# Optimization experiments

Hardware: AMD Instinct MI355X
Metric: run time of the kernel (lower is better)

## Reference

```python
import jax, jax.numpy as jnp
import numpy as np

H, D, VD = 8, 64, 64
QD, KD, VDIM, OUT = 512, 512, 512, 512
N, QS, VS = 16, 512, 512
TEMP = 10.0              # softstair_temp
SCALING = D ** -0.5


def _softstair(x):
    fl = jnp.floor(x)
    return fl + jax.nn.sigmoid(TEMP * (jnp.abs(x - fl) - 0.5))


def setup_inputs() -> dict:
    key = jax.random.key(0)
    ks = jax.random.split(key, 24)
    f = jax.random.normal
    s = 0.03  # xavier-ish scale
    return {
        "Q": f(ks[0], (N, QS, QD), jnp.float32),
        "K": f(ks[1], (N, VS, KD), jnp.float32),
        "V": f(ks[2], (N, VS, VDIM), jnp.float32),
        "past_state": f(ks[3], (N, H, QS, D), jnp.float32),
        "past_attention": jax.random.uniform(ks[4], (N, H, QS, 1), jnp.float32),
        "value_positions": jnp.arange(VS, dtype=jnp.float32),
        "attention_mask": jnp.ones((N, QS, VS), jnp.int32),
        "Wq": f(ks[5], (QD, H * D), jnp.float32) * s,
        "Wk": f(ks[6], (KD, H * D), jnp.float32) * s,
        "Wv": f(ks[7], (VDIM, H * VD), jnp.float32) * s,
        "Wpos": f(ks[8], (QD, H * D), jnp.float32) * s,
        "bpos": f(ks[9], (H * D,), jnp.float32) * s,
        "Wsigma": f(ks[10], (H, D, 1), jnp.float32) * s,
        "Wrho": f(ks[11], (H, D, 3), jnp.float32) * s,
        "mix_w": f(ks[12], (QD, 1), jnp.float32) * s,
        "mix_b": f(ks[13], (1,), jnp.float32) * s,
        "gru_wi": f(ks[14], (D, 3 * D), jnp.float32) * s,
        "gru_wh": f(ks[15], (D, 3 * D), jnp.float32) * s,
        "gru_bi": f(ks[16], (3 * D,), jnp.float32) * s,
        "gru_bh": f(ks[17], (3 * D,), jnp.float32) * s,
        "Wc": f(ks[18], (H * VD, OUT), jnp.float32) * s,
    }


def reference(Q, K, V, past_state, past_attention, value_positions, attention_mask,
              Wq, Wk, Wv, Wpos, bpos, Wsigma, Wrho, mix_w, mix_b,
              gru_wi, gru_wh, gru_bi, gru_bh, Wc):
    n, qS, _ = Q.shape
    vS = K.shape[1]
    mask_f = attention_mask.astype(jnp.float32)          # [N,qS,vS]
    mask_b = attention_mask.astype(bool)[:, None]        # [N,1,qS,vS]
    lengths = jnp.sum(mask_f, axis=-1)                   # [N,qS]
    l_1 = jnp.maximum(1.0, lengths - 1.0)[:, None, :, None]
    step_size = 1.0 / l_1                                # [N,1,qS,1]
    nvp = value_positions[None, None, None, :] * step_size  # [N,1,qS,vS]

    # mix gate
    mix = jax.nn.sigmoid(Q @ mix_w + mix_b)[:, None]     # [N,1,qS,1]

    # projections -> [N,H,S,d]
    Qpos = (Q @ Wpos + bpos).reshape(n, qS, H, D).transpose(0, 2, 1, 3)
    Qh = (Q @ Wq).reshape(n, qS, H, D).transpose(0, 2, 1, 3)
    Kh = (K @ Wk).reshape(n, vS, H, D).transpose(0, 2, 1, 3)
    Vh = (V @ Wv).reshape(n, vS, H, VD).transpose(0, 2, 1, 3)

    # content attention
    content = jnp.einsum('bhqd,bhkd->bhqk', Qh, Kh) * SCALING
    content_attn = jax.nn.softmax(jnp.where(mask_b, content, -jnp.inf), axis=-1)

    # GRUCell update (torch gate order r,z,n) on relu(Qpos) with past_state
    x = jax.nn.relu(Qpos)
    gi = x @ gru_wi + gru_bi
    gh = past_state @ gru_wh + gru_bh
    ir, iz, inn = jnp.split(gi, 3, axis=-1)
    hr, hz, hn = jnp.split(gh, 3, axis=-1)
    r = jax.nn.sigmoid(ir + hr)
    z = jax.nn.sigmoid(iz + hz)
    nn_ = jnp.tanh(inn + r * hn)
    state = (1.0 - z) * nn_ + z * past_state             # [N,H,qS,D]

    # location (Gaussian) attention
    sigma = (jax.nn.relu(jnp.einsum('bhqd,hde->bhqe', state, Wsigma)) + 0.27) \
            / lengths[:, None, :, None]                  # [N,H,qS,1]
    rho = jnp.einsum('bhqd,hde->bhqe', state, Wrho)      # [N,H,qS,3]
    steps = _softstair(rho[..., 0:1])
    attn_gate = jax.nn.sigmoid(rho[..., 1:2])
    bias_gate = jax.nn.sigmoid(rho[..., 2:3])
    mu_ = steps * step_size + attn_gate * past_attention + bias_gate
    # leaky clamp to [0,1]
    mu = jnp.maximum(0.01 * mu_, jnp.minimum(mu_, 1.0 + 0.01 * mu_))
    diff = nvp - mu                                      # [N,H,qS,vS]
    gauss = jnp.exp(-(diff * diff) / (2.0 * sigma * sigma))
    g = gauss * mask_f[:, None]
    pos_attn = g / jnp.sum(g + 1e-20, axis=-1, keepdims=True)

    scores = mix * pos_attn + (1.0 - mix) * content_attn
    attended = jnp.einsum('bhqk,bhkv->bhqv', scores, Vh)
    out = attended.transpose(0, 2, 1, 3).reshape(n, qS, H * VD) @ Wc
    return out
```

## Files before the change

### kernel.cpp

```cpp
#include <hip/hip_runtime.h>


typedef __bf16 bf16;
typedef __bf16 bfx8 __attribute__((ext_vector_type(8)));
typedef float v4f __attribute__((ext_vector_type(4)));

__device__ inline float sigm(float x) { return 1.0f / (1.0f + __expf(-x)); }

__device__ inline v4f mfma16(bfx8 a, bfx8 b, v4f c) {
    return __builtin_amdgcn_mfma_f32_16x16x32_bf16(a, b, c, 0, 0, 0);
}

__device__ inline void split8(const float* __restrict__ p, bfx8& hi, bfx8& lo) {
    float4 x = *(const float4*)p;
    float4 y = *(const float4*)(p + 4);
    float v[8] = {x.x, x.y, x.z, x.w, y.x, y.y, y.z, y.w};
#pragma unroll
    for (int j = 0; j < 8; ++j) {
        bf16 h = (bf16)v[j];
        hi[j] = h;
        lo[j] = (bf16)(v[j] - (float)h);
    }
}

__global__ __launch_bounds__(256) void conv_qkv_kernel(
    const float* __restrict__ s0, const float* __restrict__ s1, const float* __restrict__ s2,
    bf16* __restrict__ d0, bf16* __restrict__ d1, bf16* __restrict__ d2) {
    int tb = blockIdx.x >> 11;
    const float* src = tb == 0 ? s0 : (tb == 1 ? s1 : s2);
    bf16* dst = tb == 0 ? d0 : (tb == 1 ? d1 : d2);
    long i0 = (long)(blockIdx.x & 2047) * 2048 + threadIdx.x * 8;
    float4 x = *(const float4*)(src + i0);
    float4 y = *(const float4*)(src + i0 + 4);
    bfx8 o;
    o[0] = (bf16)x.x; o[1] = (bf16)x.y; o[2] = (bf16)x.z; o[3] = (bf16)x.w;
    o[4] = (bf16)y.x; o[5] = (bf16)y.y; o[6] = (bf16)y.z; o[7] = (bf16)y.w;
    *(bfx8*)(dst + i0) = o;
}

struct TW { const float* src[5]; bf16* dst[5]; bf16* dstlo[5]; };

__global__ __launch_bounds__(256) void trans_w_kernel(TW a) {
    __shared__ float tile[64][68];
    const float* src = a.src[blockIdx.y];
    bf16* dst = a.dst[blockIdx.y];
    bf16* dlo = a.dstlo[blockIdx.y];
    const int rbase = (blockIdx.x >> 3) * 64, cbase = (blockIdx.x & 7) * 64;
    const int t = threadIdx.x;
    const int r = t >> 2, cc = (t & 3) * 16;
    {
        const float* p = src + (long)(rbase + r) * 512 + cbase + cc;
        *(float4*)(&tile[r][cc]) = *(const float4*)p;
        *(float4*)(&tile[r][cc + 4]) = *(const float4*)(p + 4);
        *(float4*)(&tile[r][cc + 8]) = *(const float4*)(p + 8);
        *(float4*)(&tile[r][cc + 12]) = *(const float4*)(p + 12);
    }
    __syncthreads();
    {
        bfx8 h0, h1, l0, l1;
#pragma unroll
        for (int j = 0; j < 8; ++j) {
            float v0 = tile[cc + j][r];
            float v1 = tile[cc + 8 + j][r];
            bf16 a0 = (bf16)v0, a1 = (bf16)v1;
            h0[j] = a0; l0[j] = (bf16)(v0 - (float)a0);
            h1[j] = a1; l1[j] = (bf16)(v1 - (float)a1);
        }
        bf16* p = dst + (long)(cbase + r) * 512 + rbase + cc;
        *(bfx8*)p = h0;
        *(bfx8*)(p + 8) = h1;
        if (dlo) {
            bf16* pl = dlo + (long)(cbase + r) * 512 + rbase + cc;
            *(bfx8*)pl = l0;
            *(bfx8*)(pl + 8) = l1;
        }
    }
}

__global__ void gru_prep_kernel(const float* __restrict__ gwi, const float* __restrict__ gwh,
                                bf16* ih, bf16* il, bf16* hh, bf16* hl) {
    const float* src = blockIdx.x ? gwh : gwi;
    bf16* dh = blockIdx.x ? hh : ih;
    bf16* dl = blockIdx.x ? hl : il;
    int n = threadIdx.x;
    for (int k = 0; k < 64; ++k) {
        float v = src[k * 192 + n];
        bf16 h = (bf16)v;
        dh[n * 64 + k] = h;
        dl[n * 64 + k] = (bf16)(v - (float)h);
    }
}

struct G3 { const bf16* A[3]; const bf16* BT[3]; bf16* C[3]; };

__global__ __launch_bounds__(256) void gemm_bt3(G3 g) {
    __shared__ bf16 As[64][72];
    __shared__ bf16 Bs[64][72];

    const int z = blockIdx.z;
    const bf16* __restrict__ A = g.A[z];
    const bf16* __restrict__ BT = g.BT[z];
    bf16* __restrict__ C = g.C[z];

    const int mbase = blockIdx.x * 64, nbase = blockIdx.y * 64;
    const int t = threadIdx.x;
    const int wave = t >> 6, lane = t & 63;
    const int quad = lane >> 4, c = lane & 15;
    const int wrow = (wave >> 1) * 32, wcol = (wave & 1) * 32;

    const v4f zero4 = {0.f, 0.f, 0.f, 0.f};
    v4f acc[2][2];
    acc[0][0] = zero4; acc[0][1] = zero4; acc[1][0] = zero4; acc[1][1] = zero4;

    const int sr = t >> 2, sch = t & 3;

    for (int k0 = 0; k0 < 512; k0 += 32) {
        bfx8 va = *(const bfx8*)(A + (long)(mbase + sr) * 512 + k0 + sch * 8);
        bfx8 vb = *(const bfx8*)(BT + (long)(nbase + sr) * 512 + k0 + sch * 8);
        *(bfx8*)(&As[sr][sch * 8]) = va;
        *(bfx8*)(&Bs[sr][sch * 8]) = vb;
        __syncthreads();

        bfx8 a0 = *(const bfx8*)(&As[wrow + c][quad * 8]);
        bfx8 a1 = *(const bfx8*)(&As[wrow + 16 + c][quad * 8]);
        bfx8 b0 = *(const bfx8*)(&Bs[wcol + c][quad * 8]);
        bfx8 b1 = *(const bfx8*)(&Bs[wcol + 16 + c][quad * 8]);
        acc[0][0] = mfma16(a0, b0, acc[0][0]);
        acc[0][1] = mfma16(a0, b1, acc[0][1]);
        acc[1][0] = mfma16(a1, b0, acc[1][0]);
        acc[1][1] = mfma16(a1, b1, acc[1][1]);
        __syncthreads();
    }

    if (z == 2) {
#pragma unroll
        for (int tm = 0; tm < 2; ++tm)
#pragma unroll
            for (int tn = 0; tn < 2; ++tn)
#pragma unroll
                for (int i = 0; i < 4; ++i) {
                    int rl = wrow + tm * 16 + quad * 4 + i;
                    int cl = wcol + tn * 16 + c;
                    As[cl][rl] = (bf16)acc[tm][tn][i];
                }
        __syncthreads();
        bf16* CT = C + ((long)(mbase >> 9)) * 262144 + (long)nbase * 512 + (mbase & 511);
        const int rr = t >> 2, kc = (t & 3) * 16;
        bfx8 o0, o1;
#pragma unroll
        for (int j = 0; j < 8; ++j) { o0[j] = As[rr][kc + j]; o1[j] = As[rr][kc + 8 + j]; }
        *(bfx8*)(CT + (long)rr * 512 + kc) = o0;
        *(bfx8*)(CT + (long)rr * 512 + kc + 8) = o1;
    } else {
#pragma unroll
        for (int tm = 0; tm < 2; ++tm)
#pragma unroll
            for (int tn = 0; tn < 2; ++tn)
#pragma unroll
                for (int i = 0; i < 4; ++i) {
                    int row = mbase + wrow + tm * 16 + quad * 4 + i;
                    int col = nbase + wcol + tn * 16 + c;
                    C[(long)row * 512 + col] = (bf16)acc[tm][tn][i];
                }
    }
}

__global__ __launch_bounds__(256) void gemm_out(
    const bf16* __restrict__ A, const bf16* __restrict__ BT, float* __restrict__ C) {
    __shared__ bf16 As[64][72];
    __shared__ bf16 Bs[64][72];

    const int mbase = blockIdx.x * 64, nbase = blockIdx.y * 64;
    const int t = threadIdx.x;
    const int wave = t >> 6, lane = t & 63;
    const int quad = lane >> 4, c = lane & 15;
    const int wrow = (wave >> 1) * 32, wcol = (wave & 1) * 32;

    const v4f zero4 = {0.f, 0.f, 0.f, 0.f};
    v4f acc[2][2];
    acc[0][0] = zero4; acc[0][1] = zero4; acc[1][0] = zero4; acc[1][1] = zero4;

    const int sr = t >> 2, sch = t & 3;

    for (int k0 = 0; k0 < 512; k0 += 32) {
        bfx8 va = *(const bfx8*)(A + (long)(mbase + sr) * 512 + k0 + sch * 8);
        bfx8 vb = *(const bfx8*)(BT + (long)(nbase + sr) * 512 + k0 + sch * 8);
        *(bfx8*)(&As[sr][sch * 8]) = va;
        *(bfx8*)(&Bs[sr][sch * 8]) = vb;
        __syncthreads();

        bfx8 a0 = *(const bfx8*)(&As[wrow + c][quad * 8]);
        bfx8 a1 = *(const bfx8*)(&As[wrow + 16 + c][quad * 8]);
        bfx8 b0 = *(const bfx8*)(&Bs[wcol + c][quad * 8]);
        bfx8 b1 = *(const bfx8*)(&Bs[wcol + 16 + c][quad * 8]);
        acc[0][0] = mfma16(a0, b0, acc[0][0]);
        acc[0][1] = mfma16(a0, b1, acc[0][1]);
        acc[1][0] = mfma16(a1, b0, acc[1][0]);
        acc[1][1] = mfma16(a1, b1, acc[1][1]);
        __syncthreads();
    }

#pragma unroll
    for (int tm = 0; tm < 2; ++tm)
#pragma unroll
        for (int tn = 0; tn < 2; ++tn)
#pragma unroll
            for (int i = 0; i < 4; ++i) {
                int row = mbase + wrow + tm * 16 + quad * 4 + i;
                int col = nbase + wcol + tn * 16 + c;
                C[(long)row * 512 + col] = acc[tm][tn][i];
            }
}

__global__ __launch_bounds__(256) void gemm_split_hl(
    const float* __restrict__ A, const bf16* __restrict__ BTh,
    const bf16* __restrict__ BTl, const float* __restrict__ bias,
    bf16* __restrict__ Ch, bf16* __restrict__ Cl) {
    __shared__ bf16 Ah[64][72], Al[64][72];
    __shared__ bf16 Bh[64][72], Bl[64][72];

    const int mbase = blockIdx.x * 64, nbase = blockIdx.y * 64;
    const int t = threadIdx.x;
    const int wave = t >> 6, lane = t & 63;
    const int quad = lane >> 4, c = lane & 15;
    const int wrow = (wave >> 1) * 32, wcol = (wave & 1) * 32;

    const v4f zero4 = {0.f, 0.f, 0.f, 0.f};
    v4f acc[2][2];
    acc[0][0] = zero4; acc[0][1] = zero4; acc[1][0] = zero4; acc[1][1] = zero4;

    const int sr = t >> 2, sch = t & 3;

    for (int k0 = 0; k0 < 512; k0 += 32) {
        bfx8 h, l;
        split8(A + (long)(mbase + sr) * 512 + k0 + sch * 8, h, l);
        *(bfx8*)(&Ah[sr][sch * 8]) = h;
        *(bfx8*)(&Al[sr][sch * 8]) = l;
        *(bfx8*)(&Bh[sr][sch * 8]) = *(const bfx8*)(BTh + (long)(nbase + sr) * 512 + k0 + sch * 8);
        *(bfx8*)(&Bl[sr][sch * 8]) = *(const bfx8*)(BTl + (long)(nbase + sr) * 512 + k0 + sch * 8);
        __syncthreads();

        bfx8 ah0 = *(const bfx8*)(&Ah[wrow + c][quad * 8]);
        bfx8 ah1 = *(const bfx8*)(&Ah[wrow + 16 + c][quad * 8]);
        bfx8 al0 = *(const bfx8*)(&Al[wrow + c][quad * 8]);
        bfx8 al1 = *(const bfx8*)(&Al[wrow + 16 + c][quad * 8]);
        bfx8 bh0 = *(const bfx8*)(&Bh[wcol + c][quad * 8]);
        bfx8 bh1 = *(const bfx8*)(&Bh[wcol + 16 + c][quad * 8]);
        bfx8 bl0 = *(const bfx8*)(&Bl[wcol + c][quad * 8]);
        bfx8 bl1 = *(const bfx8*)(&Bl[wcol + 16 + c][quad * 8]);
        acc[0][0] = mfma16(ah0, bh0, acc[0][0]);
        acc[0][0] = mfma16(ah0, bl0, acc[0][0]);
        acc[0][0] = mfma16(al0, bh0, acc[0][0]);
        acc[0][1] = mfma16(ah0, bh1, acc[0][1]);
        acc[0][1] = mfma16(ah0, bl1, acc[0][1]);
        acc[0][1] = mfma16(al0, bh1, acc[0][1]);
        acc[1][0] = mfma16(ah1, bh0, acc[1][0]);
        acc[1][0] = mfma16(ah1, bl0, acc[1][0]);
        acc[1][0] = mfma16(al1, bh0, acc[1][0]);
        acc[1][1] = mfma16(ah1, bh1, acc[1][1]);
        acc[1][1] = mfma16(ah1, bl1, acc[1][1]);
        acc[1][1] = mfma16(al1, bh1, acc[1][1]);
        __syncthreads();
    }

#pragma unroll
    for (int tm = 0; tm < 2; ++tm)
#pragma unroll
        for (int tn = 0; tn < 2; ++tn)
#pragma unroll
            for (int i = 0; i < 4; ++i) {
                int row = mbase + wrow + tm * 16 + quad * 4 + i;
                int col = nbase + wcol + tn * 16 + c;
                float v = fmaxf(acc[tm][tn][i] + bias[col], 0.f);
                bf16 h = (bf16)v;
                Ch[(long)row * 512 + col] = h;
                Cl[(long)row * 512 + col] = (bf16)(v - (float)h);
            }
}

__global__ __launch_bounds__(256) void mix_len_kernel(
    const float* __restrict__ Q, const int* __restrict__ mask,
    const float* __restrict__ mix_w, const float* __restrict__ mix_b,
    float* __restrict__ mixv, float* __restrict__ stepv, float* __restrict__ lenv,
    unsigned* __restrict__ maskbits) {
    int row = blockIdx.x * 4 + (threadIdx.x >> 6);
    int lane = threadIdx.x & 63;
    float dot = 0.f, ms = 0.f;
    unsigned myw = 0;
#pragma unroll
    for (int j = 0; j < 8; ++j) {
        float qv = Q[(long)row * 512 + j * 64 + lane];
        float wv = mix_w[j * 64 + lane];
        dot += qv * wv;
        int mv = mask[(long)row * 512 + j * 64 + lane];
        unsigned long long b = __ballot(mv != 0);
        ms += (float)__popcll(b);
        if ((lane >> 1) == j) myw = (unsigned)(b >> ((lane & 1) * 32));
    }
#pragma unroll
    for (int o = 32; o > 0; o >>= 1) dot += __shfl_xor(dot, o);
    if (lane < 16) maskbits[(long)row * 16 + lane] = myw;
    if (lane == 0) {
        mixv[row] = sigm(dot + mix_b[0]);
        lenv[row] = ms;
        stepv[row] = 1.0f / fmaxf(1.0f, ms - 1.0f);
    }
}

__global__ __launch_bounds__(256) void gru_fused_kernel(
    const bf16* __restrict__ Xh, const bf16* __restrict__ Xl,
    const float* __restrict__ hp,
    const bf16* __restrict__ wih, const bf16* __restrict__ wil,
    const bf16* __restrict__ whh, const bf16* __restrict__ whl,
    const float* __restrict__ gbi, const float* __restrict__ gbh,
    const float* __restrict__ pa, const float* __restrict__ Wsigma,
    const float* __restrict__ Wrho,
    const float* __restrict__ lenv, const float* __restrict__ stepv,
    float* __restrict__ muv, float* __restrict__ sigv) {
    __shared__ bf16 Wh[192][72], Wl[192][72];
    __shared__ float biL[384];

    const int b = blockIdx.x;
    const int qb = b & 7, nh = b >> 3, hd = nh & 7, n = nh >> 3;
    const int t = threadIdx.x;
    const int w = t >> 6, lane = t & 63, quad = lane >> 4, c = lane & 15;
    const int q0 = qb * 64 + w * 16;

    if (t < 192) { biL[t] = gbi[t]; biL[192 + t] = gbh[t]; }
#pragma unroll
    for (int it = 0; it < 6; ++it) {
        int task = it * 256 + t;
        int r = task >> 3, ch = task & 7;
        *(bfx8*)(&Wh[r][ch * 8]) = *(const bfx8*)(wih + r * 64 + ch * 8);
        *(bfx8*)(&Wl[r][ch * 8]) = *(const bfx8*)(wil + r * 64 + ch * 8);
    }
    __syncthreads();

    const v4f zero4 = {0.f, 0.f, 0.f, 0.f};
    v4f gi[12], gh[12];
#pragma unroll
    for (int nt = 0; nt < 12; ++nt) gi[nt] = zero4;
#pragma unroll
    for (int ks = 0; ks < 2; ++ks) {
        long ao = (long)(n * 512 + q0 + c) * 512 + hd * 64 + ks * 32 + quad * 8;
        bfx8 xh = *(const bfx8*)(Xh + ao);
        bfx8 xl = *(const bfx8*)(Xl + ao);
#pragma unroll
        for (int nt = 0; nt < 12; ++nt) {
            bfx8 bh = *(const bfx8*)(&Wh[nt * 16 + c][ks * 32 + quad * 8]);
            bfx8 bl = *(const bfx8*)(&Wl[nt * 16 + c][ks * 32 + quad * 8]);
            gi[nt] = mfma16(xh, bh, gi[nt]);
            gi[nt] = mfma16(xh, bl, gi[nt]);
            gi[nt] = mfma16(xl, bh, gi[nt]);
        }
    }
    __syncthreads();
#pragma unroll
    for (int it = 0; it < 6; ++it) {
        int task = it * 256 + t;
        int r = task >> 3, ch = task & 7;
        *(bfx8*)(&Wh[r][ch * 8]) = *(const bfx8*)(whh + r * 64 + ch * 8);
        *(bfx8*)(&Wl[r][ch * 8]) = *(const bfx8*)(whl + r * 64 + ch * 8);
    }
    __syncthreads();
#pragma unroll
    for (int nt = 0; nt < 12; ++nt) gh[nt] = zero4;
#pragma unroll
    for (int ks = 0; ks < 2; ++ks) {
        bfx8 ah, al;
        split8(hp + (long)(nh * 512 + q0 + c) * 64 + ks * 32 + quad * 8, ah, al);
#pragma unroll
        for (int nt = 0; nt < 12; ++nt) {
            bfx8 bh = *(const bfx8*)(&Wh[nt * 16 + c][ks * 32 + quad * 8]);
            bfx8 bl = *(const bfx8*)(&Wl[nt * 16 + c][ks * 32 + quad * 8]);
            gh[nt] = mfma16(ah, bh, gh[nt]);
            gh[nt] = mfma16(ah, bl, gh[nt]);
            gh[nt] = mfma16(al, bh, gh[nt]);
        }
    }

    float st[4][4];
#pragma unroll
    for (int t4 = 0; t4 < 4; ++t4) {
        float bir = biL[t4 * 16 + c];
        float biz = biL[64 + t4 * 16 + c];
        float bin = biL[128 + t4 * 16 + c];
        float bhr = biL[192 + t4 * 16 + c];
        float bhz = biL[256 + t4 * 16 + c];
        float bhn = biL[320 + t4 * 16 + c];
#pragma unroll
        for (int i = 0; i < 4; ++i) {
            int row = q0 + quad * 4 + i;
            float r = sigm(gi[t4][i] + bir + gh[t4][i] + bhr);
            float z = sigm(gi[t4 + 4][i] + biz + gh[t4 + 4][i] + bhz);
            float nn_ = tanhf(gi[t4 + 8][i] + bin + r * (gh[t4 + 8][i] + bhn));
            float hpv = hp[(long)(nh * 512 + row) * 64 + t4 * 16 + c];
            st[t4][i] = (1.0f - z) * nn_ + z * hpv;
        }
    }

    float ws_[4], wr0[4], wr1[4], wr2[4];
#pragma unroll
    for (int t4 = 0; t4 < 4; ++t4) {
        int d = t4 * 16 + c;
        ws_[t4] = Wsigma[hd * 64 + d];
        wr0[t4] = Wrho[(hd * 64 + d) * 3 + 0];
        wr1[t4] = Wrho[(hd * 64 + d) * 3 + 1];
        wr2[t4] = Wrho[(hd * 64 + d) * 3 + 2];
    }
#pragma unroll
    for (int i = 0; i < 4; ++i) {
        float s0 = 0.f, s1 = 0.f, s2 = 0.f, s3 = 0.f;
#pragma unroll
        for (int t4 = 0; t4 < 4; ++t4) {
            float sv = st[t4][i];
            s0 += sv * ws_[t4];
            s1 += sv * wr0[t4];
            s2 += sv * wr1[t4];
            s3 += sv * wr2[t4];
        }
#pragma unroll
        for (int o = 1; o < 16; o <<= 1) {
            s0 += __shfl_xor(s0, o);
            s1 += __shfl_xor(s1, o);
            s2 += __shfl_xor(s2, o);
            s3 += __shfl_xor(s3, o);
        }
        if (c == 0) {
            int row = q0 + quad * 4 + i;
            int idx = nh * 512 + row, rq = n * 512 + row;
            float L = lenv[rq], sp = stepv[rq];
            float sg = (fmaxf(s0, 0.f) + 0.27f) / L;
            float fl = floorf(s1);
            float steps = fl + sigm(10.0f * (fabsf(s1 - fl) - 0.5f));
            float ag = sigm(s2), bg = sigm(s3);
            float mu_ = steps * sp + ag * pa[idx] + bg;
            float mu = fmaxf(0.01f * mu_, fminf(mu_, 1.0f + 0.01f * mu_));
            muv[idx] = mu;
            sigv[idx] = sg;
        }
    }
}

__global__ __launch_bounds__(256) void attn_fused_kernel(
    const bf16* __restrict__ Qh, const bf16* __restrict__ Kh,
    const bf16* __restrict__ VhT, const unsigned* __restrict__ maskbits,
    const float* __restrict__ vpos, const float* __restrict__ mixv,
    const float* __restrict__ stepv, const float* __restrict__ muv,
    const float* __restrict__ sigv, bf16* __restrict__ att) {
    __shared__ bf16 Plds[16][520];
    __shared__ float vps[512];
    __shared__ unsigned mb[16][16];
    __shared__ float rmax[4][16], rsum[4][16], rgsum[4][16];
    __shared__ float rowmu[16], rowsig[16], rowstep[16], rowmix[16];

    const int b = blockIdx.x;
    const int qt = b & 31, nh = b >> 5, hd = nh & 7, n = nh >> 3;
    const int t = threadIdx.x;

    if (t < 16) {
        int q = qt * 16 + t;
        int idx = nh * 512 + q, rq = n * 512 + q;
        rowmu[t] = muv[idx];
        rowsig[t] = sigv[idx];
        rowstep[t] = stepv[rq];
        rowmix[t] = mixv[rq];
    }
    vps[t] = vpos[t];
    vps[256 + t] = vpos[256 + t];
    mb[t >> 4][t & 15] = maskbits[(long)(n * 512 + qt * 16 + (t >> 4)) * 16 + (t & 15)];

    const int wave = t >> 6, lane = t & 63;
    const int quad = lane >> 4, c = lane & 15;
    const int qloc = quad * 4;

    const bf16* qrow = Qh + (long)(n * 512 + qt * 16 + c) * 512 + hd * 64 + quad * 8;
    bfx8 afr0 = *(const bfx8*)qrow;
    bfx8 afr1 = *(const bfx8*)(qrow + 32);

    const v4f zero4 = {0.f, 0.f, 0.f, 0.f};
    v4f acc[8];
#pragma unroll
    for (int i = 0; i < 8; ++i) acc[i] = zero4;

    const bf16* kbase = Kh + (long)(n * 512 + wave * 128 + c) * 512 + hd * 64 + quad * 8;
#pragma unroll
    for (int t8 = 0; t8 < 8; ++t8) {
        bfx8 b0 = *(const bfx8*)(kbase + (long)t8 * 16 * 512);
        bfx8 b1 = *(const bfx8*)(kbase + (long)t8 * 16 * 512 + 32);
        acc[t8] = mfma16(afr0, b0, acc[t8]);
        acc[t8] = mfma16(afr1, b1, acc[t8]);
    }
#pragma unroll
    for (int t8 = 0; t8 < 8; ++t8) acc[t8] = acc[t8] * 0.125f;

    __syncthreads();

    unsigned mbits[4] = {0u, 0u, 0u, 0u};
#pragma unroll
    for (int t8 = 0; t8 < 8; ++t8) {
        int wd = wave * 4 + (t8 >> 1);
        int bit = (t8 & 1) * 16 + c;
#pragma unroll
        for (int i = 0; i < 4; ++i)
            mbits[i] |= ((mb[qloc + i][wd] >> bit) & 1u) << t8;
    }

#pragma unroll
    for (int i = 0; i < 4; ++i) {
        float mx = -3.0e38f;
#pragma unroll
        for (int t8 = 0; t8 < 8; ++t8)
            if ((mbits[i] >> t8) & 1u) mx = fmaxf(mx, acc[t8][i]);
        mx = fmaxf(mx, __shfl_xor(mx, 1));
        mx = fmaxf(mx, __shfl_xor(mx, 2));
        mx = fmaxf(mx, __shfl_xor(mx, 4));
        mx = fmaxf(mx, __shfl_xor(mx, 8));
        if (c == 0) rmax[wave][qloc + i] = mx;
    }
    __syncthreads();

    float gmx[4], inv2s[4];
#pragma unroll
    for (int i = 0; i < 4; ++i) {
        gmx[i] = fmaxf(fmaxf(rmax[0][qloc + i], rmax[1][qloc + i]),
                       fmaxf(rmax[2][qloc + i], rmax[3][qloc + i]));
        float sg = rowsig[qloc + i];
        inv2s[i] = 0.5f / (sg * sg);
    }

    float psum[4] = {0.f, 0.f, 0.f, 0.f};
    float gsum[4] = {0.f, 0.f, 0.f, 0.f};
#pragma unroll
    for (int t8 = 0; t8 < 8; ++t8) {
        int k = wave * 128 + t8 * 16 + c;
        float vp = vps[k];
#pragma unroll
        for (int i = 0; i < 4; ++i) {
            int on = (mbits[i] >> t8) & 1;
            float pv = on ? __expf(acc[t8][i] - gmx[i]) : 0.f;
            float d = vp * rowstep[qloc + i] - rowmu[qloc + i];
            float gv = on ? __expf(-(d * d) * inv2s[i]) : 0.f;
            psum[i] += pv;
            gsum[i] += gv;
        }
    }
#pragma unroll
    for (int i = 0; i < 4; ++i) {
#pragma unroll
        for (int o = 1; o < 16; o <<= 1) {
            psum[i] += __shfl_xor(psum[i], o);
            gsum[i] += __shfl_xor(gsum[i], o);
        }
        if (c == 0) {
            rsum[wave][qloc + i] = psum[i];
            rgsum[wave][qloc + i] = gsum[i];
        }
    }
    __syncthreads();

    float ac[4], bc[4];
#pragma unroll
    for (int i = 0; i < 4; ++i) {
        float Sp = rsum[0][qloc + i] + rsum[1][qloc + i] + rsum[2][qloc + i] + rsum[3][qloc + i];
        float Sg = rgsum[0][qloc + i] + rgsum[1][qloc + i] + rgsum[2][qloc + i] +
                   rgsum[3][qloc + i] + 512.0f * 1e-20f;
        float m_ = rowmix[qloc + i];
        ac[i] = (1.0f - m_) / Sp;
        bc[i] = m_ / Sg;
    }

#pragma unroll
    for (int t8 = 0; t8 < 8; ++t8) {
        int k = wave * 128 + t8 * 16 + c;
        float vp = vps[k];
#pragma unroll
        for (int i = 0; i < 4; ++i) {
            int on = (mbits[i] >> t8) & 1;
            float pv = on ? __expf(acc[t8][i] - gmx[i]) : 0.f;
            float d = vp * rowstep[qloc + i] - rowmu[qloc + i];
            float gv = on ? __expf(-(d * d) * inv2s[i]) : 0.f;
            Plds[qloc + i][k] = (bf16)(pv * ac[i] + gv * bc[i]);
        }
    }
    __syncthreads();

    v4f accO = zero4;
    const bf16* vrow = VhT + (long)(n * 512 + hd * 64 + wave * 16 + c) * 512 + quad * 8;
#pragma unroll
    for (int ks = 0; ks < 16; ++ks) {
        bfx8 af = *(const bfx8*)(&Plds[c][ks * 32 + quad * 8]);
        bfx8 bf_ = *(const bfx8*)(vrow + ks * 32);
        accO = mfma16(af, bf_, accO);
    }

#pragma unroll
    for (int i = 0; i < 4; ++i) {
        att[(long)(n * 512 + qt * 16 + quad * 4 + i) * 512 + hd * 64 + wave * 16 + c] =
            (bf16)accO[i];
    }
}

extern "C" void kernel_launch(void* const* d_in, const int* in_sizes, int n_in,
                              void* d_out, int out_size, void* d_ws, size_t ws_size,
                              hipStream_t stream) {
    (void)in_sizes; (void)n_in; (void)out_size; (void)ws_size;

    const float* Q = (const float*)d_in[0];
    const float* K = (const float*)d_in[1];
    const float* V = (const float*)d_in[2];
    const float* past_state = (const float*)d_in[3];
    const float* past_att = (const float*)d_in[4];
    const float* vpos = (const float*)d_in[5];
    const int* mask = (const int*)d_in[6];
    const float* Wq = (const float*)d_in[7];
    const float* Wk = (const float*)d_in[8];
    const float* Wv = (const float*)d_in[9];
    const float* Wpos = (const float*)d_in[10];
    const float* bpos = (const float*)d_in[11];
    const float* Wsigma = (const float*)d_in[12];
    const float* Wrho = (const float*)d_in[13];
    const float* mix_w = (const float*)d_in[14];
    const float* mix_b = (const float*)d_in[15];
    const float* gwi = (const float*)d_in[16];
    const float* gwh = (const float*)d_in[17];
    const float* gbi = (const float*)d_in[18];
    const float* gbh = (const float*)d_in[19];
    const float* Wc = (const float*)d_in[20];
    float* out = (float*)d_out;

    char* p = (char*)d_ws;
    const size_t SZB = 8192UL * 512 * 2;
    const size_t SZW = 512UL * 512 * 2;
    bf16* Qc = (bf16*)p;    p += SZB;
    bf16* Kc = (bf16*)p;    p += SZB;
    bf16* Vc = (bf16*)p;    p += SZB;
    bf16* WqT = (bf16*)p;   p += SZW;
    bf16* WkT = (bf16*)p;   p += SZW;
    bf16* WvT = (bf16*)p;   p += SZW;
    bf16* WpT = (bf16*)p;   p += SZW;
    bf16* WpTl = (bf16*)p;  p += SZW;
    bf16* WcT = (bf16*)p;   p += SZW;
    bf16* wih = (bf16*)p;   p += 24576;
    bf16* wil = (bf16*)p;   p += 24576;
    bf16* whh = (bf16*)p;   p += 24576;
    bf16* whl = (bf16*)p;   p += 24576;
    bf16* Qh = (bf16*)p;    p += SZB;
    bf16* Kh = (bf16*)p;    p += SZB;
    bf16* VhT = (bf16*)p;   p += SZB;
    bf16* Xh = (bf16*)p;
    bf16* att = Xh;         p += SZB;
    bf16* Xl = (bf16*)p;    p += SZB;
    unsigned* maskbits = (unsigned*)p;   p += 8192UL * 16 * 4;
    float* mixv = (float*)p;  p += 32768;
    float* stepv = (float*)p; p += 32768;
    float* lenv = (float*)p;  p += 32768;
    float* muv = (float*)p;   p += 262144;
    float* sigv = (float*)p;  p += 262144;

    dim3 blk(256);
    dim3 gProj(128, 8, 1);

    conv_qkv_kernel<<<dim3(6144), blk, 0, stream>>>(Q, K, V, Qc, Kc, Vc);

    TW tw;
    tw.src[0] = Wq; tw.src[1] = Wk; tw.src[2] = Wv; tw.src[3] = Wpos; tw.src[4] = Wc;
    tw.dst[0] = WqT; tw.dst[1] = WkT; tw.dst[2] = WvT; tw.dst[3] = WpT; tw.dst[4] = WcT;
    tw.dstlo[0] = nullptr; tw.dstlo[1] = nullptr; tw.dstlo[2] = nullptr;
    tw.dstlo[3] = WpTl; tw.dstlo[4] = nullptr;
    trans_w_kernel<<<dim3(64, 5), blk, 0, stream>>>(tw);

    gru_prep_kernel<<<dim3(2), dim3(192), 0, stream>>>(gwi, gwh, wih, wil, whh, whl);

    G3 g;
    g.A[0] = Qc; g.A[1] = Kc; g.A[2] = Vc;
    g.BT[0] = WqT; g.BT[1] = WkT; g.BT[2] = WvT;
    g.C[0] = Qh; g.C[1] = Kh; g.C[2] = VhT;
    gemm_bt3<<<dim3(128, 8, 3), blk, 0, stream>>>(g);

    gemm_split_hl<<<gProj, blk, 0, stream>>>(Q, WpT, WpTl, bpos, Xh, Xl);

    mix_len_kernel<<<dim3(2048), blk, 0, stream>>>(Q, mask, mix_w, mix_b, mixv, stepv, lenv, maskbits);

    gru_fused_kernel<<<dim3(1024), blk, 0, stream>>>(
        Xh, Xl, past_state, wih, wil, whh, whl, gbi, gbh, past_att, Wsigma, Wrho,
        lenv, stepv, muv, sigv);

    attn_fused_kernel<<<dim3(4096), blk, 0, stream>>>(
        Qh, Kh, VhT, maskbits, vpos, mixv, stepv, muv, sigv, att);

    gemm_out<<<gProj, blk, 0, stream>>>(att, WcT, out);
}
```

Before: 365.9 us.

## Fuse fp32-to-bf16 conversion into QKV GEMM, cache attention values, fast tanh

Removes the separate conversion kernel and instead converts fp32 Q/K/V to bf16 inside the projection GEMM's tile loads, saving a full round trip of activations through memory. In the attention kernel, the softmax and Gaussian values from the first pass are kept in registers as packed bf16 rather than recomputed with exp in the second pass. This raises register pressure and adds bf16 rounding before the final mix. The attention block index mapping is reordered so consecutive blocks cover different heads of the same batch. A cheaper exp-based tanh replaces tanhf in the GRU.

Result: no change. 361.6 us (-1.2%).

```diff
diff --git a/kernel.cpp b/kernel.cpp
--- a/kernel.cpp
+++ b/kernel.cpp
@@ -6,6 +6,7 @@
 typedef float v4f __attribute__((ext_vector_type(4)));
 
 __device__ inline float sigm(float x) { return 1.0f / (1.0f + __expf(-x)); }
+__device__ inline float tanh_fast(float x) { return 1.0f - 2.0f / (__expf(2.0f * x) + 1.0f); }
 
 __device__ inline v4f mfma16(bfx8 a, bfx8 b, v4f c) {
     return __builtin_amdgcn_mfma_f32_16x16x32_bf16(a, b, c, 0, 0, 0);
@@ -23,19 +24,21 @@
     }
 }
 
-__global__ __launch_bounds__(256) void conv_qkv_kernel(
-    const float* __restrict__ s0, const float* __restrict__ s1, const float* __restrict__ s2,
-    bf16* __restrict__ d0, bf16* __restrict__ d1, bf16* __restrict__ d2) {
-    int tb = blockIdx.x >> 11;
-    const float* src = tb == 0 ? s0 : (tb == 1 ? s1 : s2);
-    bf16* dst = tb == 0 ? d0 : (tb == 1 ? d1 : d2);
-    long i0 = (long)(blockIdx.x & 2047) * 2048 + threadIdx.x * 8;
-    float4 x = *(const float4*)(src + i0);
-    float4 y = *(const float4*)(src + i0 + 4);
+__device__ inline bfx8 cvt8(const float* __restrict__ p) {
+    float4 x = *(const float4*)p;
+    float4 y = *(const float4*)(p + 4);
     bfx8 o;
     o[0] = (bf16)x.x; o[1] = (bf16)x.y; o[2] = (bf16)x.z; o[3] = (bf16)x.w;
     o[4] = (bf16)y.x; o[5] = (bf16)y.y; o[6] = (bf16)y.z; o[7] = (bf16)y.w;
-    *(bfx8*)(dst + i0) = o;
+    return o;
+}
+
+__device__ inline unsigned short bfbits(float v) {
+    bf16 h = (bf16)v;
+    return __builtin_bit_cast(unsigned short, h);
+}
+__device__ inline float bffrom(unsigned short u) {
+    return (float)__builtin_bit_cast(bf16, u);
 }
 
 struct TW { const float* src[5]; bf16* dst[5]; bf16* dstlo[5]; };
@@ -91,14 +94,14 @@
     }
 }
 
-struct G3 { const bf16* A[3]; const bf16* BT[3]; bf16* C[3]; };
+struct G3 { const float* A[3]; const bf16* BT[3]; bf16* C[3]; };
 
 __global__ __launch_bounds__(256) void gemm_bt3(G3 g) {
     __shared__ bf16 As[64][72];
     __shared__ bf16 Bs[64][72];
 
     const int z = blockIdx.z;
-    const bf16* __restrict__ A = g.A[z];
+    const float* __restrict__ A = g.A[z];
     const bf16* __restrict__ BT = g.BT[z];
     bf16* __restrict__ C = g.C[z];
 
@@ -115,7 +118,7 @@
     const int sr = t >> 2, sch = t & 3;
 
     for (int k0 = 0; k0 < 512; k0 += 32) {
-        bfx8 va = *(const bfx8*)(A + (long)(mbase + sr) * 512 + k0 + sch * 8);
+        bfx8 va = cvt8(A + (long)(mbase + sr) * 512 + k0 + sch * 8);
         bfx8 vb = *(const bfx8*)(BT + (long)(nbase + sr) * 512 + k0 + sch * 8);
         *(bfx8*)(&As[sr][sch * 8]) = va;
         *(bfx8*)(&Bs[sr][sch * 8]) = vb;
@@ -393,7 +396,7 @@
             int row = q0 + quad * 4 + i;
             float r = sigm(gi[t4][i] + bir + gh[t4][i] + bhr);
             float z = sigm(gi[t4 + 4][i] + biz + gh[t4 + 4][i] + bhz);
-            float nn_ = tanhf(gi[t4 + 8][i] + bin + r * (gh[t4 + 8][i] + bhn));
+            float nn_ = tanh_fast(gi[t4 + 8][i] + bin + r * (gh[t4 + 8][i] + bhn));
             float hpv = hp[(long)(nh * 512 + row) * 64 + t4 * 16 + c];
             st[t4][i] = (1.0f - z) * nn_ + z * hpv;
         }
@@ -455,7 +458,9 @@
     __shared__ float rowmu[16], rowsig[16], rowstep[16], rowmix[16];
 
     const int b = blockIdx.x;
-    const int qt = b & 31, nh = b >> 5, hd = nh & 7, n = nh >> 3;
+    const int nh = ((b >> 8) << 3) | (b & 7);
+    const int qt = (b >> 3) & 31;
+    const int hd = nh & 7, n = nh >> 3;
     const int t = threadIdx.x;
 
     if (t < 16) {
@@ -531,6 +536,7 @@
 
     float psum[4] = {0.f, 0.f, 0.f, 0.f};
     float gsum[4] = {0.f, 0.f, 0.f, 0.f};
+    unsigned pg[8][4];
 #pragma unroll
     for (int t8 = 0; t8 < 8; ++t8) {
         int k = wave * 128 + t8 * 16 + c;
@@ -543,6 +549,7 @@
             float gv = on ? __expf(-(d * d) * inv2s[i]) : 0.f;
             psum[i] += pv;
             gsum[i] += gv;
+            pg[t8][i] = ((unsigned)bfbits(gv) << 16) | (unsigned)bfbits(pv);
         }
     }
 #pragma unroll
@@ -573,13 +580,10 @@
 #pragma unroll
     for (int t8 = 0; t8 < 8; ++t8) {
         int k = wave * 128 + t8 * 16 + c;
-        float vp = vps[k];
 #pragma unroll
         for (int i = 0; i < 4; ++i) {
-            int on = (mbits[i] >> t8) & 1;
-            float pv = on ? __expf(acc[t8][i] - gmx[i]) : 0.f;
-            float d = vp * rowstep[qloc + i] - rowmu[qloc + i];
-            float gv = on ? __expf(-(d * d) * inv2s[i]) : 0.f;
+            float pv = bffrom((unsigned short)(pg[t8][i] & 0xffffu));
+            float gv = bffrom((unsigned short)(pg[t8][i] >> 16));
             Plds[qloc + i][k] = (bf16)(pv * ac[i] + gv * bc[i]);
         }
     }
@@ -632,9 +636,6 @@
     char* p = (char*)d_ws;
     const size_t SZB = 8192UL * 512 * 2;
     const size_t SZW = 512UL * 512 * 2;
-    bf16* Qc = (bf16*)p;    p += SZB;
-    bf16* Kc = (bf16*)p;    p += SZB;
-    bf16* Vc = (bf16*)p;    p += SZB;
     bf16* WqT = (bf16*)p;   p += SZW;
     bf16* WkT = (bf16*)p;   p += SZW;
     bf16* WvT = (bf16*)p;   p += SZW;
@@ -661,8 +662,6 @@
     dim3 blk(256);
     dim3 gProj(128, 8, 1);
 
-    conv_qkv_kernel<<<dim3(6144), blk, 0, stream>>>(Q, K, V, Qc, Kc, Vc);
-
     TW tw;
     tw.src[0] = Wq; tw.src[1] = Wk; tw.src[2] = Wv; tw.src[3] = Wpos; tw.src[4] = Wc;
     tw.dst[0] = WqT; tw.dst[1] = WkT; tw.dst[2] = WvT; tw.dst[3] = WpT; tw.dst[4] = WcT;
@@ -673,7 +672,7 @@
     gru_prep_kernel<<<dim3(2), dim3(192), 0, stream>>>(gwi, gwh, wih, wil, whh, whl);
 
     G3 g;
-    g.A[0] = Qc; g.A[1] = Kc; g.A[2] = Vc;
+    g.A[0] = Q; g.A[1] = K; g.A[2] = V;
     g.BT[0] = WqT; g.BT[1] = WkT; g.BT[2] = WvT;
     g.C[0] = Qh; g.C[1] = Kh; g.C[2] = VhT;
     gemm_bt3<<<dim3(128, 8, 3), blk, 0, stream>>>(g);
```
